# Kernel optimization log

Measured on AMD Instinct MI355X. Metric: run time of the kernel, lower is better.

## Reference

```python
import jax, jax.numpy as jnp
import numpy as np

N = 262144          # number of query points
NUM_AXES = 4        # input_dim + 2
RES = 512           # axis_resolution
EMB = 256           # embedding_dim
OUT = 3             # output_dim
W0 = 30.0           # Sine frequency


def setup_inputs() -> dict:
    key = jax.random.key(0)
    k_c, k_t, k_w1, k_b1, k_w2, k_b2 = jax.random.split(key, 6)
    coords = jax.random.uniform(k_c, (N, 2), jnp.float32, minval=-1.0, maxval=1.0)
    tables = jax.random.normal(k_t, (NUM_AXES, RES, EMB), jnp.float32) * 0.1
    # decoder: Linear(256,256) with first_layer_sine_init, Sine(30), Linear(256,3) with frequency_init(30)
    W1 = jax.random.uniform(k_w1, (256, EMB), jnp.float32, minval=-1.0 / EMB, maxval=1.0 / EMB)
    b1 = jax.random.uniform(k_b1, (256,), jnp.float32, minval=-0.0625, maxval=0.0625)
    lim2 = np.sqrt(6.0 / 256.0) / W0
    W2 = jax.random.uniform(k_w2, (OUT, 256), jnp.float32, minval=-lim2, maxval=lim2)
    b2 = jax.random.uniform(k_b2, (OUT,), jnp.float32, minval=-0.0625, maxval=0.0625)
    return {"coords": coords, "tables": tables, "W1": W1, "b1": b1, "W2": W2, "b2": b2}


def reference(coords, tables, W1, b1, W2, b2):
    # clamp input coords to [-1,1], build the 4 axis coordinates
    c = jnp.clip(coords, -1.0, 1.0)
    c = jnp.concatenate(
        [c, (c[:, 0:1] + c[:, 1:2]) * 0.5, (c[:, 0:1] - c[:, 1:2]) * 0.5], axis=-1
    )  # [N, 4]
    # linearInterpolate (vectorized over all axes at once)
    c = jnp.clip(c, -1.0, 0.999)
    t = (0.5 * c + 0.5) * (tables.shape[1] - 1)       # [N, 4] continuous index
    i0 = jnp.floor(t).astype(jnp.int32)               # [N, 4]
    w = (t - i0)[..., None]                           # [N, 4, 1]
    ax = jnp.arange(tables.shape[0])[None, :]         # [1, 4]
    v0 = tables[ax, i0]                               # [N, 4, EMB] gather
    v1 = tables[ax, i0 + 1]                           # [N, 4, EMB] gather
    emb = jnp.mean((1.0 - w) * v0 + w * v1, axis=1)   # [N, EMB] mean over axes
    # decoder: Linear -> Sine(30) -> Linear
    h = jnp.sin(W0 * (emb @ W1.T + b1))               # [N, 256]
    return h @ W2.T + b2                              # [N, 3]
```

## Files before the change

### kernel.cpp

```cpp
#include <hip/hip_runtime.h>
#include <hip/hip_bf16.h>
#include <hip/hip_fp16.h>

#define NPTS 262144
#define EMB  256
#define RES  512
#define NROWS (4 * RES)

typedef _Float16 half_t;
typedef __attribute__((ext_vector_type(8))) _Float16 half8;

__global__ __launch_bounds__(256) void t2_precompute_kernel(
    const float* __restrict__ tables,
    const float* __restrict__ W1,
    half_t* __restrict__ T2)
{
    __shared__ __align__(16) float arow[8][EMB];
    const int row0 = blockIdx.x * 8;
    const int o = threadIdx.x;

    #pragma unroll
    for (int r = 0; r < 8; ++r)
        arow[r][o] = tables[(row0 + r) * EMB + o];
    __syncthreads();

    float acc[8] = {0.f, 0.f, 0.f, 0.f, 0.f, 0.f, 0.f, 0.f};
    const float4* __restrict__ w1v = reinterpret_cast<const float4*>(W1 + o * EMB);
    for (int ec = 0; ec < EMB / 4; ++ec) {
        const float4 w4 = w1v[ec];
        #pragma unroll
        for (int r = 0; r < 8; ++r) {
            const float4 a4 = *reinterpret_cast<const float4*>(&arow[r][ec * 4]);
            acc[r] = fmaf(w4.x, a4.x, acc[r]);
            acc[r] = fmaf(w4.y, a4.y, acc[r]);
            acc[r] = fmaf(w4.z, a4.z, acc[r]);
            acc[r] = fmaf(w4.w, a4.w, acc[r]);
        }
    }
    const float s = 7.5f * 0.15915494309189535f;
    #pragma unroll
    for (int r = 0; r < 8; ++r)
        T2[(row0 + r) * EMB + o] = (half_t)(s * acc[r]);
}

__global__ __launch_bounds__(256) void eval_kernel(
    const float* __restrict__ coords,
    const half_t* __restrict__ T2,
    const float* __restrict__ b1,
    const float* __restrict__ W2,
    const float* __restrict__ b2,
    float* __restrict__ out)
{
    const int lane = threadIdx.x & 63;
    const int g    = lane >> 4;
    const int l16  = lane & 15;
    const int e0   = l16 * 16;

    const int wave   = blockIdx.x * 4 + (threadIdx.x >> 6);
    const int nwaves = gridDim.x * 4;

    const float sb = 30.f * 0.15915494309189535f;
    float bias[16];
    #pragma unroll
    for (int d = 0; d < 16; ++d) bias[d] = sb * b1[e0 + d];

    half8 w2h[3][2];
    #pragma unroll
    for (int j = 0; j < 3; ++j)
        #pragma unroll
        for (int k = 0; k < 2; ++k)
            #pragma unroll
            for (int i = 0; i < 8; ++i)
                w2h[j][k][i] = (half_t)W2[j * EMB + e0 + k * 8 + i];

    const float ob0 = b2[0], ob1 = b2[1], ob2 = b2[2];
    const char* __restrict__ T2b = reinterpret_cast<const char*>(T2);

    for (int pq = wave; pq < NPTS / 4; pq += nwaves) {
        const int p = 4 * pq + g;
        const float2 cf = *reinterpret_cast<const float2*>(coords + 2 * p);
        const float x = fminf(fmaxf(cf.x, -1.f), 1.f);
        const float y = fminf(fmaxf(cf.y, -1.f), 1.f);

        half8 accA = {0, 0, 0, 0, 0, 0, 0, 0};
        half8 accB = {0, 0, 0, 0, 0, 0, 0, 0};

        #pragma unroll
        for (int a = 0; a < 4; ++a) {
            float c = (a == 0) ? x : (a == 1) ? y
                    : (a == 2) ? 0.5f * (x + y) : 0.5f * (x - y);
            c = fminf(fmaxf(c, -1.f), 0.999f);
            const float t  = fmaf(c, 255.5f, 255.5f);
            const float fi = floorf(t);
            const float w  = t - fi;
            const half_t hw   = (half_t)w;
            const half_t homw = (half_t)(1.f - w);
            const char* base = T2b + ((((a << 9) + (int)fi) << 9) + (e0 << 1));
            const half8 v0a = *reinterpret_cast<const half8*>(base);
            const half8 v0b = *reinterpret_cast<const half8*>(base + 16);
            const half8 v1a = *reinterpret_cast<const half8*>(base + 512);
            const half8 v1b = *reinterpret_cast<const half8*>(base + 528);
            accA = v0a * homw + accA;
            accA = v1a * hw   + accA;
            accB = v0b * homw + accB;
            accB = v1b * hw   + accB;
        }

        float q0 = 0.f, q1 = 0.f, q2 = 0.f;
        #pragma unroll
        for (int d = 0; d < 16; ++d) {
            const half_t a16 = (d < 8) ? accA[d] : accB[d - 8];
            const float arg = fmaf((float)a16, 1.0f, bias[d]);
            const float h = __builtin_amdgcn_sinf(__builtin_amdgcn_fractf(arg));
            q0 = fmaf(h, (float)w2h[0][d >> 3][d & 7], q0);
            q1 = fmaf(h, (float)w2h[1][d >> 3][d & 7], q1);
            q2 = fmaf(h, (float)w2h[2][d >> 3][d & 7], q2);
        }

        #pragma unroll
        for (int off = 8; off > 0; off >>= 1) {
            q0 += __shfl_xor(q0, off, 64);
            q1 += __shfl_xor(q1, off, 64);
            q2 += __shfl_xor(q2, off, 64);
        }

        if (l16 == 0) {
            out[3 * p + 0] = q0 + ob0;
            out[3 * p + 1] = q1 + ob1;
            out[3 * p + 2] = q2 + ob2;
        }
    }
}

extern "C" void kernel_launch(void* const* d_in, const int* in_sizes, int n_in,
                              void* d_out, int out_size, void* d_ws, size_t ws_size,
                              hipStream_t stream) {
    const float* coords = (const float*)d_in[0];
    const float* tables = (const float*)d_in[1];
    const float* W1     = (const float*)d_in[2];
    const float* b1     = (const float*)d_in[3];
    const float* W2     = (const float*)d_in[4];
    const float* b2     = (const float*)d_in[5];
    float* out = (float*)d_out;

    half_t* T2 = (half_t*)d_ws;

    hipLaunchKernelGGL(t2_precompute_kernel, dim3(NROWS / 8), dim3(256), 0, stream,
                       tables, W1, T2);
    hipLaunchKernelGGL(eval_kernel, dim3(2048), dim3(256), 0, stream,
                       coords, T2, b1, W2, b2, out);
}
```

Before: 66.36 us.

## Coalesce table gathers, batch loads, fold bias into fp16, use fdot2 output

Each lane of a 16-lane group now owns two 8-element slices, 128 elements apart, instead of one contiguous 16-element slice. This makes every 16-byte gather instruction read contiguous memory across lanes. All 16 row loads per point are issued before any FMA to raise memory-level parallelism. The bias is pre-added in the fp16 accumulator and the fract range reduction is dropped. The 256-to-3 output projection uses packed fp16 dot2 instructions, and launch bounds request 4 blocks per CU. The fp16 bias and removing fract add small precision risk, and hoisting the loads raises register pressure.

```diff
diff --git a/kernel.cpp b/kernel.cpp
--- a/kernel.cpp
+++ b/kernel.cpp
@@ -9,6 +9,7 @@
 
 typedef _Float16 half_t;
 typedef __attribute__((ext_vector_type(8))) _Float16 half8;
+typedef __attribute__((ext_vector_type(2))) _Float16 half2v;
 
 __global__ __launch_bounds__(256) void t2_precompute_kernel(
     const float* __restrict__ tables,
@@ -43,7 +44,7 @@
         T2[(row0 + r) * EMB + o] = (half_t)(s * acc[r]);
 }
 
-__global__ __launch_bounds__(256) void eval_kernel(
+__global__ __launch_bounds__(256, 4) void eval_kernel(
     const float* __restrict__ coords,
     const half_t* __restrict__ T2,
     const float* __restrict__ b1,
@@ -54,27 +55,31 @@
     const int lane = threadIdx.x & 63;
     const int g    = lane >> 4;
     const int l16  = lane & 15;
-    const int e0   = l16 * 16;
+    const int dA   = l16 * 8;
+    const int dB   = 128 + l16 * 8;
 
     const int wave   = blockIdx.x * 4 + (threadIdx.x >> 6);
     const int nwaves = gridDim.x * 4;
 
     const float sb = 30.f * 0.15915494309189535f;
-    float bias[16];
+    half8 biasA, biasB;
     #pragma unroll
-    for (int d = 0; d < 16; ++d) bias[d] = sb * b1[e0 + d];
-
-    half8 w2h[3][2];
+    for (int i = 0; i < 8; ++i) {
+        biasA[i] = (half_t)(sb * b1[dA + i]);
+        biasB[i] = (half_t)(sb * b1[dB + i]);
+    }
+    half2v w2p[3][8];
     #pragma unroll
     for (int j = 0; j < 3; ++j)
         #pragma unroll
-        for (int k = 0; k < 2; ++k)
-            #pragma unroll
-            for (int i = 0; i < 8; ++i)
-                w2h[j][k][i] = (half_t)W2[j * EMB + e0 + k * 8 + i];
-
+        for (int k = 0; k < 4; ++k) {
+            w2p[j][k][0]     = (half_t)W2[j * EMB + dA + 2 * k];
+            w2p[j][k][1]     = (half_t)W2[j * EMB + dA + 2 * k + 1];
+            w2p[j][4 + k][0] = (half_t)W2[j * EMB + dB + 2 * k];
+            w2p[j][4 + k][1] = (half_t)W2[j * EMB + dB + 2 * k + 1];
+        }
     const float ob0 = b2[0], ob1 = b2[1], ob2 = b2[2];
-    const char* __restrict__ T2b = reinterpret_cast<const char*>(T2);
+    const char* __restrict__ T2b = reinterpret_cast<const char*>(T2) + (l16 << 4);
 
     for (int pq = wave; pq < NPTS / 4; pq += nwaves) {
         const int p = 4 * pq + g;
@@ -82,9 +87,8 @@
         const float x = fminf(fmaxf(cf.x, -1.f), 1.f);
         const float y = fminf(fmaxf(cf.y, -1.f), 1.f);
 
-        half8 accA = {0, 0, 0, 0, 0, 0, 0, 0};
-        half8 accB = {0, 0, 0, 0, 0, 0, 0, 0};
-
+        int rb[4];
+        half_t hw[4], homw[4];
         #pragma unroll
         for (int a = 0; a < 4; ++a) {
             float c = (a == 0) ? x : (a == 1) ? y
@@ -93,28 +97,60 @@
             const float t  = fmaf(c, 255.5f, 255.5f);
             const float fi = floorf(t);
             const float w  = t - fi;
-            const half_t hw   = (half_t)w;
-            const half_t homw = (half_t)(1.f - w);
-            const char* base = T2b + ((((a << 9) + (int)fi) << 9) + (e0 << 1));
-            const half8 v0a = *reinterpret_cast<const half8*>(base);
-            const half8 v0b = *reinterpret_cast<const half8*>(base + 16);
-            const half8 v1a = *reinterpret_cast<const half8*>(base + 512);
-            const half8 v1b = *reinterpret_cast<const half8*>(base + 528);
-            accA = v0a * homw + accA;
-            accA = v1a * hw   + accA;
-            accB = v0b * homw + accB;
-            accB = v1b * hw   + accB;
+            hw[a]   = (half_t)w;
+            homw[a] = (half_t)(1.f - w);
+            rb[a]   = (((a << 9) + (int)fi) << 9);
+        }
+
+        half8 A0[4], B0[4], A1[4], B1[4];
+        #pragma unroll
+        for (int a = 0; a < 4; ++a) {
+            const char* base = T2b + rb[a];
+            A0[a] = *reinterpret_cast<const half8*>(base);
+            B0[a] = *reinterpret_cast<const half8*>(base + 256);
+            A1[a] = *reinterpret_cast<const half8*>(base + 512);
+            B1[a] = *reinterpret_cast<const half8*>(base + 768);
+        }
+
+        half8 accA = biasA, accB = biasB;
+        #pragma unroll
+        for (int a = 0; a < 4; ++a) {
+            accA = A0[a] * homw[a] + accA;
+            accA = A1[a] * hw[a]   + accA;
+            accB = B0[a] * homw[a] + accB;
+            accB = B1[a] * hw[a]   + accB;
         }
 
         float q0 = 0.f, q1 = 0.f, q2 = 0.f;
         #pragma unroll
-        for (int d = 0; d < 16; ++d) {
-            const half_t a16 = (d < 8) ? accA[d] : accB[d - 8];
-            const float arg = fmaf((float)a16, 1.0f, bias[d]);
-            const float h = __builtin_amdgcn_sinf(__builtin_amdgcn_fractf(arg));
-            q0 = fmaf(h, (float)w2h[0][d >> 3][d & 7], q0);
-            q1 = fmaf(h, (float)w2h[1][d >> 3][d & 7], q1);
-            q2 = fmaf(h, (float)w2h[2][d >> 3][d & 7], q2);
+        for (int k = 0; k < 4; ++k) {
+            const float s0 = __builtin_amdgcn_sinf((float)accA[2 * k]);
+            const float s1 = __builtin_amdgcn_sinf((float)accA[2 * k + 1]);
+#if __has_builtin(__builtin_amdgcn_fdot2)
+            const half2v hp = __builtin_bit_cast(half2v, __builtin_amdgcn_cvt_pkrtz(s0, s1));
+            q0 = __builtin_amdgcn_fdot2(hp, w2p[0][k], q0, false);
+            q1 = __builtin_amdgcn_fdot2(hp, w2p[1][k], q1, false);
+            q2 = __builtin_amdgcn_fdot2(hp, w2p[2][k], q2, false);
+#else
+            q0 = fmaf(s0, (float)w2p[0][k][0], fmaf(s1, (float)w2p[0][k][1], q0));
+            q1 = fmaf(s0, (float)w2p[1][k][0], fmaf(s1, (float)w2p[1][k][1], q1));
+            q2 = fmaf(s0, (float)w2p[2][k][0], fmaf(s1, (float)w2p[2][k][1], q2));
+#endif
+        }
+        #pragma unroll
+        for (int k = 0; k < 4; ++k) {
+            const float s0 = __builtin_amdgcn_sinf((float)accB[2 * k]);
+            const float s1 = __builtin_amdgcn_sinf((float)accB[2 * k + 1]);
+#if __has_builtin(__builtin_amdgcn_fdot2)
+            const half2v hp = __builtin_bit_cast(half2v, __builtin_amdgcn_cvt_pkrtz(s0, s1));
+            q0 = __builtin_amdgcn_fdot2(hp, w2p[0][4 + k], q0, false);
+            q1 = __builtin_amdgcn_fdot2(hp, w2p[1][4 + k], q1, false);
+            q2 = __builtin_amdgcn_fdot2(hp, w2p[2][4 + k], q2, false);
+#else
+            q0 = fmaf(s0, (float)w2p[0][4 + k][0], fmaf(s1, (float)w2p[0][4 + k][1], q0));
+            q1 = fmaf(s0, (float)w2p[1][4 + k][0], fmaf(s1, (float)w2p[1][4 + k][1], q1));
+            q2 = fmaf(s0, (float)w2p[2][4 + k][0], fmaf(s1, (float)w2p[2][4 + k][1], q2));
+#endif
         }
 
         #pragma unroll
```

After: 59.62 us. -10.2%, faster.
